# Performance work log

Measured on AMD Instinct MI355X. Metric: run time of the kernel, lower is better.

Reference implementation:

```python
import jax, jax.numpy as jnp
import numpy as np

D = 1024          # model_dim
BD = D // 2       # bottleneck_dim
K = 64            # num_splats
B, S = 8, 2048


def setup_inputs() -> dict:
    key = jax.random.key(0)
    ks = jax.random.split(key, 12)
    sc = 0.02
    return {
        "token_embeddings": jax.random.normal(ks[0], (B, S, D), jnp.float32),
        "splat_influences": jax.random.uniform(ks[1], (B, S, K), jnp.float32),
        # encoder: Linear(D -> BD), stored [in, out]
        "enc_W": jax.random.normal(ks[2], (D, BD), jnp.float32) * sc,
        "enc_b": jnp.zeros((BD,), jnp.float32),
        # per-splat transforms: K x Linear(BD -> BD)
        "trans_W": jax.random.normal(ks[3], (K, BD, BD), jnp.float32) * sc,
        "trans_b": jnp.zeros((K, BD), jnp.float32),
        # decoder: Linear(BD -> D)
        "dec_W": jax.random.normal(ks[4], (BD, D), jnp.float32) * sc,
        "dec_b": jnp.zeros((D,), jnp.float32),
        # flow gate: Linear(D -> D) + sigmoid
        "gate_W": jax.random.normal(ks[5], (D, D), jnp.float32) * sc,
        "gate_b": jnp.zeros((D,), jnp.float32),
    }


def reference(token_embeddings, splat_influences, enc_W, enc_b,
              trans_W, trans_b, dec_W, dec_b, gate_W, gate_b):
    # gather: [B,K,S] @ [B,S,D] -> [B,K,D]
    influences_t = jnp.swapaxes(splat_influences, 1, 2)          # [B,K,S]
    gathered = jnp.einsum('bks,bsd->bkd', influences_t, token_embeddings)
    total = jnp.clip(influences_t.sum(axis=2, keepdims=True), 1e-8, None)  # [B,K,1]
    gathered = gathered / total
    # encoder (dropout inactive at eval)
    encoded = jax.nn.relu(gathered @ enc_W + enc_b)              # [B,K,BD]
    # per-splat transform as grouped matmul
    transformed = jnp.einsum('bkd,kde->bke', encoded, trans_W) + trans_b  # [B,K,BD]
    decoded = transformed @ dec_W + dec_b                        # [B,K,D]
    # scatter back to tokens: [B,S,K] @ [B,K,D]
    flow = jnp.einsum('bsk,bkd->bsd', splat_influences, decoded)
    gate = jax.nn.sigmoid(token_embeddings @ gate_W + gate_b)    # [B,S,D]
    return flow * gate
```

## Files before the change

kernel.cpp:

```cpp
#include <hip/hip_runtime.h>

#define BB 8
#define SS 2048
#define DD 1024
#define BDD 512
#define NSP 64

typedef __attribute__((ext_vector_type(8))) short bf16x8;
typedef __attribute__((ext_vector_type(4))) float f32x4;
typedef unsigned short u16;
typedef unsigned int u32;

__device__ __forceinline__ u16 f2bf(float f) {
  u32 u = __builtin_bit_cast(u32, f);
  u = u + 0x7fffu + ((u >> 16) & 1u);
  return (u16)(u >> 16);
}

__device__ __forceinline__ void gl_lds16(const void* g, void* l) {
  __builtin_amdgcn_global_load_lds((const __attribute__((address_space(1))) void*)g,
                                   (__attribute__((address_space(3))) void*)l,
                                   16, 0, 0);
}

__global__ void k_prep(const float* __restrict__ infl, const float* __restrict__ gw,
                       u16* __restrict__ inflbf, u16* __restrict__ inflT,
                       float* __restrict__ rsum, u16* __restrict__ gwt) {
  __shared__ __align__(16) char smraw[64 * 80 * 2 + 32 * 64 * 4];
  u16(*tile)[80] = (u16(*)[80])smraw;
  float(*ps)[64] = (float(*)[64])(smraw + 64 * 80 * 2);
  float(*gt)[33] = (float(*)[33])smraw;
  int bid = blockIdx.x;
  int t = threadIdx.x;

  if (bid < 256) {
    int R0 = bid * 64;
    int b = R0 >> 11, s0 = R0 & 2047;
    int st = s0 >> 6;
    int lr = t >> 3, lc = (t & 7) * 8;
    float col[8];
#pragma unroll
    for (int j = 0; j < 8; ++j) col[j] = 0.f;
#pragma unroll
    for (int i = 0; i < 2; ++i) {
      int r = lr + i * 32;
      const float* src = infl + (size_t)(R0 + r) * NSP + lc;
      float4 a = *(const float4*)src;
      float4 bq = *(const float4*)(src + 4);
      col[0] += a.x; col[1] += a.y; col[2] += a.z; col[3] += a.w;
      col[4] += bq.x; col[5] += bq.y; col[6] += bq.z; col[7] += bq.w;
      uint4 v;
      v.x = f2bf(a.x) | ((u32)f2bf(a.y) << 16);
      v.y = f2bf(a.z) | ((u32)f2bf(a.w) << 16);
      v.z = f2bf(bq.x) | ((u32)f2bf(bq.y) << 16);
      v.w = f2bf(bq.z) | ((u32)f2bf(bq.w) << 16);
      *(uint4*)(inflbf + (size_t)(R0 + r) * NSP + lc) = v;
      *(uint4*)&tile[r][lc] = v;
    }
#pragma unroll
    for (int j = 0; j < 8; ++j) ps[lr][lc + j] = col[j];
    __syncthreads();
    if (t < 64) {
      float s = 0.f;
#pragma unroll
      for (int rr = 0; rr < 32; ++rr) s += ps[rr][t];
      rsum[((size_t)b * 32 + st) * 64 + t] = s;
    }
    int sseg = (t & 7) * 8;
    size_t ibase = (size_t)b * NSP * SS + (size_t)st * (NSP * 64);
#pragma unroll
    for (int i = 0; i < 2; ++i) {
      int dcol = (t >> 3) + i * 32;
      u16 a0 = tile[sseg + 0][dcol], a1 = tile[sseg + 1][dcol];
      u16 a2 = tile[sseg + 2][dcol], a3 = tile[sseg + 3][dcol];
      u16 a4 = tile[sseg + 4][dcol], a5 = tile[sseg + 5][dcol];
      u16 a6 = tile[sseg + 6][dcol], a7 = tile[sseg + 7][dcol];
      uint4 v;
      v.x = a0 | ((u32)a1 << 16);
      v.y = a2 | ((u32)a3 << 16);
      v.z = a4 | ((u32)a5 << 16);
      v.w = a6 | ((u32)a7 << 16);
      *(uint4*)(inflT + ibase + (size_t)dcol * 64 + sseg) = v;
    }
  } else {
    int g = bid - 256;
    int n0 = (g & 31) * 32, k0 = (g >> 5) * 32;
    int tx = t & 31, ty = t >> 5;
#pragma unroll
    for (int r = 0; r < 4; ++r) {
      int kr = ty + r * 8;
      gt[kr][tx] = gw[(k0 + kr) * DD + n0 + tx];
    }
    __syncthreads();
#pragma unroll
    for (int r = 0; r < 4; ++r) {
      int nc = ty + r * 8;
      gwt[(n0 + nc) * DD + k0 + tx] = f2bf(gt[tx][nc]);
    }
  }
}

__global__ __launch_bounds__(256) void k_gather_mfma(const u16* __restrict__ inflT,
                                                     const float* __restrict__ tok,
                                                     u16* __restrict__ tokbf,
                                                     float* __restrict__ pg) {
  __shared__ u16 As[64 * 64];
  __shared__ u16 Bs[64 * 64];
  int t = threadIdx.x;
  int l = t & 63, w = t >> 6;
  int wr = w >> 1, wc = w & 1;
  int n0 = blockIdx.x * 64;
  int b = blockIdx.y;
  int sq = blockIdx.z;
  int l15 = l & 15, lh = l >> 4;

  const u16* ap = inflT + (size_t)b * NSP * SS;
  int s = t >> 2;
  int dseg = (t & 3) * 16;

  f32x4 acc[2][2];
#pragma unroll
  for (int i = 0; i < 2; ++i)
#pragma unroll
    for (int j = 0; j < 2; ++j) acc[i][j] = (f32x4){0.f, 0.f, 0.f, 0.f};

  for (int kt = 0; kt < 8; ++kt) {
    int pc = sq * 8 + kt;
    const u16* app = ap + (size_t)pc * (NSP * 64);
#pragma unroll
    for (int i = 0; i < 2; ++i) {
      int e = i * 256 + t;
      int row = e >> 3;
      int cs = ((e & 7) ^ (row & 7)) * 8;
      gl_lds16(app + row * 64 + cs, &As[e * 8]);
    }
    {
      size_t off = ((size_t)(b * SS + pc * 64 + s)) * DD + n0 + dseg;
      const float* src = tok + off;
      float4 fa = *(const float4*)src;
      float4 fb = *(const float4*)(src + 4);
      float4 fc = *(const float4*)(src + 8);
      float4 fd = *(const float4*)(src + 12);
      u32 wd[8];
      wd[0] = f2bf(fa.x) | ((u32)f2bf(fa.y) << 16);
      wd[1] = f2bf(fa.z) | ((u32)f2bf(fa.w) << 16);
      wd[2] = f2bf(fb.x) | ((u32)f2bf(fb.y) << 16);
      wd[3] = f2bf(fb.z) | ((u32)f2bf(fb.w) << 16);
      wd[4] = f2bf(fc.x) | ((u32)f2bf(fc.y) << 16);
      wd[5] = f2bf(fc.z) | ((u32)f2bf(fc.w) << 16);
      wd[6] = f2bf(fd.x) | ((u32)f2bf(fd.y) << 16);
      wd[7] = f2bf(fd.z) | ((u32)f2bf(fd.w) << 16);
      uint4 v0, v1;
      v0.x = wd[0]; v0.y = wd[1]; v0.z = wd[2]; v0.w = wd[3];
      v1.x = wd[4]; v1.y = wd[5]; v1.z = wd[6]; v1.w = wd[7];
      *(uint4*)(tokbf + off) = v0;
      *(uint4*)(tokbf + off + 8) = v1;
      int shi = (s >> 3), slo = (s & 7);
#pragma unroll
      for (int p = 0; p < 8; ++p) {
        int d0 = dseg + p * 2, d1 = dseg + p * 2 + 1;
        Bs[d0 * 64 + ((shi ^ ((d0 >> 3) & 7)) * 8) + slo] = (u16)wd[p];
        Bs[d1 * 64 + ((shi ^ ((d1 >> 3) & 7)) * 8) + slo] = (u16)(wd[p] >> 16);
      }
    }
    __syncthreads();
#pragma unroll
    for (int ks = 0; ks < 2; ++ks) {
      int g = ks * 4 + lh;
      bf16x8 af[2], bfv[2];
#pragma unroll
      for (int mi = 0; mi < 2; ++mi) {
        int ar = wr * 32 + mi * 16 + l15;
        af[mi] = *(const bf16x8*)&As[ar * 64 + ((g ^ (ar & 7)) * 8)];
      }
#pragma unroll
      for (int ni = 0; ni < 2; ++ni) {
        int br = wc * 32 + ni * 16 + l15;
        bfv[ni] = *(const bf16x8*)&Bs[br * 64 + ((g ^ ((br >> 3) & 7)) * 8)];
      }
#pragma unroll
      for (int mi = 0; mi < 2; ++mi)
#pragma unroll
        for (int ni = 0; ni < 2; ++ni)
          acc[mi][ni] = __builtin_amdgcn_mfma_f32_16x16x32_bf16(af[mi], bfv[ni], acc[mi][ni], 0, 0, 0);
    }
    __syncthreads();
  }

#pragma unroll
  for (int mi = 0; mi < 2; ++mi)
#pragma unroll
    for (int ni = 0; ni < 2; ++ni)
#pragma unroll
      for (int r = 0; r < 4; ++r) {
        int krow = wr * 32 + mi * 16 + lh * 4 + r;
        int dcol = n0 + wc * 32 + ni * 16 + l15;
        pg[((size_t)sq * 512 + b * NSP + krow) * DD + dcol] = acc[mi][ni][r];
      }
}

__global__ void k_enc_part(const float* __restrict__ pg, const float* __restrict__ rsum,
                           const float* __restrict__ encW, float* __restrict__ pe) {
  __shared__ float gl[8][128];
  int dq = blockIdx.x, mt = blockIdx.y;
  int m0 = mt * 8, d0 = dq * 128;
  int t = threadIdx.x;
  {
    int r = t >> 5, c = t & 31;
    float s[4] = {0.f, 0.f, 0.f, 0.f};
#pragma unroll
    for (int q = 0; q < 4; ++q) {
      const float* qp = pg + ((size_t)q * 512 + m0 + r) * DD + d0;
      s[0] += qp[c]; s[1] += qp[c + 32]; s[2] += qp[c + 64]; s[3] += qp[c + 96];
    }
    int mrow = m0 + r;
    int bq = mrow >> 6, kq = mrow & 63;
    float tt = 0.f;
#pragma unroll
    for (int st = 0; st < 32; ++st) tt += rsum[((size_t)bq * 32 + st) * 64 + kq];
    float rt = 1.f / fmaxf(tt, 1e-8f);
    gl[r][c] = s[0] * rt;
    gl[r][c + 32] = s[1] * rt;
    gl[r][c + 64] = s[2] * rt;
    gl[r][c + 96] = s[3] * rt;
  }
  __syncthreads();
  int n4 = (t & 127) * 4, mh = (t >> 7) * 4;
  float4 acc[4];
#pragma unroll
  for (int m = 0; m < 4; ++m) acc[m] = (float4){0.f, 0.f, 0.f, 0.f};
  for (int i = 0; i < 128; ++i) {
    float4 wv = *(const float4*)(encW + (d0 + i) * BDD + n4);
#pragma unroll
    for (int m = 0; m < 4; ++m) {
      float g = gl[mh + m][i];
      acc[m].x += g * wv.x; acc[m].y += g * wv.y;
      acc[m].z += g * wv.z; acc[m].w += g * wv.w;
    }
  }
#pragma unroll
  for (int m = 0; m < 4; ++m)
    *(float4*)(pe + ((size_t)dq * 512 + m0 + mh + m) * BDD + n4) = acc[m];
}

__global__ void k_trans_part(const float* __restrict__ pe, const float* __restrict__ encB,
                             const float* __restrict__ trW, float* __restrict__ pt) {
  __shared__ float el[8][64];
  int dq = blockIdx.x, ks = blockIdx.y;
  int d0 = dq * 64;
  int t = threadIdx.x;
  {
    int r = t >> 5, c = t & 31;
    int m = r * NSP + ks;
    float s1 = 0.f, s2 = 0.f;
#pragma unroll
    for (int p = 0; p < 8; ++p) {
      const float* qp = pe + ((size_t)p * 512 + m) * BDD + d0;
      s1 += qp[c]; s2 += qp[c + 32];
    }
    el[r][c] = fmaxf(s1 + encB[d0 + c], 0.f);
    el[r][c + 32] = fmaxf(s2 + encB[d0 + c + 32], 0.f);
  }
  __syncthreads();
  int n4 = (t & 127) * 4, mh = (t >> 7) * 4;
  float4 acc[4];
#pragma unroll
  for (int m = 0; m < 4; ++m) acc[m] = (float4){0.f, 0.f, 0.f, 0.f};
  for (int i = 0; i < 64; ++i) {
    float4 wv = *(const float4*)(trW + ((size_t)ks * BDD + d0 + i) * BDD + n4);
#pragma unroll
    for (int m = 0; m < 4; ++m) {
      float g = el[mh + m][i];
      acc[m].x += g * wv.x; acc[m].y += g * wv.y;
      acc[m].z += g * wv.z; acc[m].w += g * wv.w;
    }
  }
#pragma unroll
  for (int m = 0; m < 4; ++m)
    *(float4*)(pt + ((size_t)dq * 512 + (mh + m) * NSP + ks) * BDD + n4) = acc[m];
}

__global__ void k_dec_part(const float* __restrict__ pt, const float* __restrict__ trB,
                           const float* __restrict__ decW, float* __restrict__ pd) {
  __shared__ float tl[8][64];
  int dq = blockIdx.x, mt = blockIdx.y;
  int m0 = mt * 8, d0 = dq * 64;
  int t = threadIdx.x;
  {
    int r = t >> 5, c = t & 31;
    int m = m0 + r;
    float s1 = 0.f, s2 = 0.f;
#pragma unroll
    for (int p = 0; p < 8; ++p) {
      const float* qp = pt + ((size_t)p * 512 + m) * BDD + d0;
      s1 += qp[c]; s2 += qp[c + 32];
    }
    tl[r][c] = s1 + trB[(m & 63) * BDD + d0 + c];
    tl[r][c + 32] = s2 + trB[(m & 63) * BDD + d0 + c + 32];
  }
  __syncthreads();
  int n4 = t * 4;
  float4 acc[8];
#pragma unroll
  for (int m = 0; m < 8; ++m) acc[m] = (float4){0.f, 0.f, 0.f, 0.f};
  for (int i = 0; i < 64; ++i) {
    float4 wv = *(const float4*)(decW + (d0 + i) * DD + n4);
#pragma unroll
    for (int m = 0; m < 8; ++m) {
      float g = tl[m][i];
      acc[m].x += g * wv.x; acc[m].y += g * wv.y;
      acc[m].z += g * wv.z; acc[m].w += g * wv.w;
    }
  }
#pragma unroll
  for (int m = 0; m < 8; ++m)
    *(float4*)(pd + ((size_t)dq * 512 + m0 + m) * DD + n4) = acc[m];
}

__global__ void red_dec(const float* __restrict__ pd, const float* __restrict__ decB,
                        u16* __restrict__ decT) {
  __shared__ u16 st[64][34];
  int nt = blockIdx.x, b = blockIdx.y;
  int n0 = nt * 32;
  int t = threadIdx.x;
  int nn = t & 31, kg = t >> 5;
  float db = decB[n0 + nn];
#pragma unroll
  for (int ki = 0; ki < 8; ++ki) {
    int ks = kg * 8 + ki;
    float s = db;
#pragma unroll
    for (int p = 0; p < 8; ++p)
      s += pd[((size_t)p * 512 + b * NSP + ks) * DD + n0 + nn];
    st[ks][nn] = f2bf(s);
  }
  __syncthreads();
  int nr = t >> 3, kseg = (t & 7) * 8;
  uint4 v;
  v.x = st[kseg + 0][nr] | ((u32)st[kseg + 1][nr] << 16);
  v.y = st[kseg + 2][nr] | ((u32)st[kseg + 3][nr] << 16);
  v.z = st[kseg + 4][nr] | ((u32)st[kseg + 5][nr] << 16);
  v.w = st[kseg + 6][nr] | ((u32)st[kseg + 7][nr] << 16);
  *(uint4*)(decT + ((size_t)b * DD + n0 + nr) * NSP + kseg) = v;
}


#define GVM(n) asm volatile("s_waitcnt vmcnt(" #n ")" ::: "memory");

#define GSTA(sl, k0, p)                                                        \
  { int e = (p)*512 + t; int row = e >> 3; int cs = ((e & 7) ^ (row & 7)) * 8; \
    gl_lds16(tokbf + (size_t)(m0 + row) * DD + (k0) + cs, &As[sl][e * 8]); }
#define GSTB(sl, k0, p)                                                        \
  { int e = (p)*512 + t; int row = e >> 3; int cs = ((e & 7) ^ (row & 7)) * 8; \
    gl_lds16(gwt + (size_t)(n0 + row) * DD + (k0) + cs, &Bs[sl][e * 8]); }
#define SAI(sl, p)                                                             \
  { int e = (p)*512 + t; int row = e >> 3; int cs = ((e & 7) ^ (row & 7)) * 8; \
    gl_lds16(inflbf + ((size_t)bb * SS + s0m + row) * NSP + cs, &As[sl][e * 8]); }
#define SBD(sl, p)                                                             \
  { int e = (p)*512 + t; int row = e >> 3; int cs = ((e & 7) ^ (row & 7)) * 8; \
    gl_lds16(decT + ((size_t)bb * DD + n0 + row) * NSP + cs, &Bs[sl][e * 8]); }

#define GLOADB(sl)                                                             \
  _Pragma("unroll")                                                            \
  for (int nf = 0; nf < 2; ++nf) {                                             \
    int br = wc * 32 + nf * 16 + l15;                                          \
    bfv[nf][0] = *(const bf16x8*)&Bs[sl][br * 64 + c0];                        \
    bfv[nf][1] = *(const bf16x8*)&Bs[sl][br * 64 + c1];                        \
  }

#define GPH(sl, mq, VMW, STG, LDB)                                             \
  {                                                                            \
    VMW                                                                        \
    __builtin_amdgcn_s_barrier();                                              \
    LDB                                                                        \
    bf16x8 af[4][2];                                                           \
    _Pragma("unroll")                                                          \
    for (int mf = 0; mf < 4; ++mf) {                                           \
      int ar = (mq)*64 + mf * 16 + l15;                                        \
      af[mf][0] = *(const bf16x8*)&As[sl][ar * 64 + c0];                       \
      af[mf][1] = *(const bf16x8*)&As[sl][ar * 64 + c1];                       \
    }                                                                          \
    STG                                                                        \
    __builtin_amdgcn_s_setprio(1);                                             \
    _Pragma("unroll")                                                          \
    for (int mf = 0; mf < 4; ++mf)                                             \
      _Pragma("unroll")                                                        \
      for (int nf = 0; nf < 2; ++nf) {                                         \
        acc[(mq)*4 + mf][nf] = __builtin_amdgcn_mfma_f32_16x16x32_bf16(af[mf][0], bfv[nf][0], acc[(mq)*4 + mf][nf], 0, 0, 0); \
        acc[(mq)*4 + mf][nf] = __builtin_amdgcn_mfma_f32_16x16x32_bf16(af[mf][1], bfv[nf][1], acc[(mq)*4 + mf][nf], 0, 0, 0); \
      }                                                                        \
    __builtin_amdgcn_s_setprio(0);                                             \
    __builtin_amdgcn_s_barrier();                                              \
  }

#define GT_FULL(sl, osl, k1)                                                   \
  {                                                                            \
    bf16x8 bfv[2][2];                                                          \
    GPH(sl, 0, GVM(3), GSTB(osl, k1, 0) GSTB(osl, k1, 1), GLOADB(sl))          \
    GPH(sl, 1, GVM(4), GSTB(osl, k1, 2) GSTB(osl, k1, 3), )                    \
    GPH(sl, 2, GVM(5), GSTA(osl, k1, 0) GSTA(osl, k1, 1), )                    \
    GPH(sl, 3, GVM(6), GSTA(osl, k1, 2) GSTA(osl, k1, 3), )                    \
  }
#define GT_LAST2(sl)                                                           \
  {                                                                            \
    bf16x8 bfv[2][2];                                                          \
    GPH(sl, 0, GVM(3), SAI(0, 0) SAI(0, 1), GLOADB(sl))                        \
    GPH(sl, 1, GVM(4), SAI(0, 2) SAI(0, 3), )                                  \
    GPH(sl, 2, GVM(5), SBD(0, 0) SBD(0, 1), )                                  \
    GPH(sl, 3, GVM(6), SBD(0, 2) SBD(0, 3), )                                  \
  }

__global__ __launch_bounds__(512, 1) void k_gate(const u16* __restrict__ tokbf,
                                                 const u16* __restrict__ gwt,
                                                 const u16* __restrict__ inflbf,
                                                 const u16* __restrict__ decT,
                                                 const float* __restrict__ gateB,
                                                 float* __restrict__ outp) {
  __shared__ u16 As[2][256 * 64];
  __shared__ u16 Bs[2][256 * 64];
  int t = threadIdx.x;
  int l = t & 63, wc = t >> 6;
  int bid = blockIdx.x;
  int mt = (bid & 7) * 8 + ((bid >> 3) & 7);
  int nt = bid >> 6;
  int m0 = mt * 256, n0 = nt * 256;
  int l15 = l & 15, lh = l >> 4;
  int x7 = l15 & 7;
  int c0 = (lh ^ x7) * 8;
  int c1 = ((4 + lh) ^ x7) * 8;
  int bb = m0 >> 11, s0m = m0 & 2047;

  f32x4 acc[16][2];
#pragma unroll
  for (int i = 0; i < 16; ++i)
#pragma unroll
    for (int j = 0; j < 2; ++j) acc[i][j] = (f32x4){0.f, 0.f, 0.f, 0.f};

  GSTB(0, 0, 0) GSTB(0, 0, 1) GSTB(0, 0, 2) GSTB(0, 0, 3)
  GSTA(0, 0, 0) GSTA(0, 0, 1) GSTA(0, 0, 2) GSTA(0, 0, 3)

#pragma unroll 1
  for (int i = 0; i < 7; ++i) {
    GT_FULL(0, 1, (2 * i + 1) * 64)
    GT_FULL(1, 0, (2 * i + 2) * 64)
  }
  GT_FULL(0, 1, 960)
  GT_LAST2(1)

  GVM(0)
  __builtin_amdgcn_s_barrier();

  {
    float gb[2];
#pragma unroll
    for (int nf = 0; nf < 2; ++nf) gb[nf] = gateB[n0 + wc * 32 + nf * 16 + l15];
    bf16x8 bfv[2][2];
    GLOADB(0)
#pragma unroll
    for (int mq = 0; mq < 4; ++mq) {
      bf16x8 af[4][2];
#pragma unroll
      for (int mf = 0; mf < 4; ++mf) {
        int ar = mq * 64 + mf * 16 + l15;
        af[mf][0] = *(const bf16x8*)&As[0][ar * 64 + c0];
        af[mf][1] = *(const bf16x8*)&As[0][ar * 64 + c1];
      }
      f32x4 accf[4][2];
#pragma unroll
      for (int mf = 0; mf < 4; ++mf)
#pragma unroll
        for (int nf = 0; nf < 2; ++nf) accf[mf][nf] = (f32x4){0.f, 0.f, 0.f, 0.f};
      __builtin_amdgcn_s_setprio(1);
#pragma unroll
      for (int mf = 0; mf < 4; ++mf)
#pragma unroll
        for (int nf = 0; nf < 2; ++nf) {
          accf[mf][nf] = __builtin_amdgcn_mfma_f32_16x16x32_bf16(af[mf][0], bfv[nf][0], accf[mf][nf], 0, 0, 0);
          accf[mf][nf] = __builtin_amdgcn_mfma_f32_16x16x32_bf16(af[mf][1], bfv[nf][1], accf[mf][nf], 0, 0, 0);
        }
      __builtin_amdgcn_s_setprio(0);
#pragma unroll
      for (int mf = 0; mf < 4; ++mf)
#pragma unroll
        for (int nf = 0; nf < 2; ++nf)
#pragma unroll
          for (int r = 0; r < 4; ++r) {
            int mr = m0 + (mq * 4 + mf) * 16 + lh * 4 + r;
            int nc = n0 + wc * 32 + nf * 16 + l15;
            float z = acc[mq * 4 + mf][nf][r] + gb[nf];
            float gate = 1.f / (1.f + __expf(-z));
            outp[(size_t)mr * DD + nc] = accf[mf][nf][r] * gate;
          }
    }
  }
}

extern "C" void kernel_launch(void* const* d_in, const int* in_sizes, int n_in,
                              void* d_out, int out_size, void* d_ws, size_t ws_size,
                              hipStream_t stream) {
  const float* tok = (const float*)d_in[0];
  const float* infl = (const float*)d_in[1];
  const float* encW = (const float*)d_in[2];
  const float* encB = (const float*)d_in[3];
  const float* trW = (const float*)d_in[4];
  const float* trB = (const float*)d_in[5];
  const float* decW = (const float*)d_in[6];
  const float* decB = (const float*)d_in[7];
  const float* gw = (const float*)d_in[8];
  const float* gateB = (const float*)d_in[9];
  float* outp = (float*)d_out;

  char* wsp = (char*)d_ws;
  u16* tokbf = (u16*)(wsp);
  u16* gwt = (u16*)(wsp + 33554432);
  u16* inflbf = (u16*)(wsp + 35651584);
  u16* decT = (u16*)(wsp + 41945088);
  float* pe = (float*)(wsp + 42993664);
  float* pt = (float*)(wsp + 42993664 + 8388608);
  u16* inflT = (u16*)(wsp + 76548096);
  float* rsum = (float*)(wsp + 78645248);
  float* scratch = (float*)(wsp + 78710784);

  k_prep<<<dim3(1280), dim3(256), 0, stream>>>(infl, gw, inflbf, inflT, rsum, gwt);
  k_gather_mfma<<<dim3(16, 8, 4), dim3(256), 0, stream>>>(inflT, tok, tokbf, scratch);
  k_enc_part<<<dim3(8, 64), dim3(256), 0, stream>>>(scratch, rsum, encW, pe);
  k_trans_part<<<dim3(8, 64), dim3(256), 0, stream>>>(pe, encB, trW, pt);
  k_dec_part<<<dim3(8, 64), dim3(256), 0, stream>>>(pt, trB, decW, scratch);
  red_dec<<<dim3(32, 8), dim3(256), 0, stream>>>(scratch, decB, decT);
  k_gate<<<dim3(256), dim3(512), 0, stream>>>(tokbf, gwt, inflbf, decT, gateB, outp);
}
```

Baseline: 148.1 us.

## Merge prep/gather and mid-stage kernels into cooperative launches with grid syncs

Six small kernel launches collapse into two cooperative kernels. The prep and gather stages are joined, and so are the encoder, transform, decoder and reduction stages, with cg grid syncs in place of kernel boundaries. The aim is to cut per-launch overhead and the gaps between short dependent kernels. In exchange, grid-wide barriers are added, the grid is fixed at 512 blocks, and prep work is looped over fewer blocks.

```diff
diff --git a/kernel.cpp b/kernel.cpp
--- a/kernel.cpp
+++ b/kernel.cpp
@@ -1,4 +1,7 @@
 #include <hip/hip_runtime.h>
+#include <hip/hip_cooperative_groups.h>
+
+namespace cg = cooperative_groups;
 
 #define BB 8
 #define SS 2048
@@ -23,325 +26,353 @@
                                    16, 0, 0);
 }
 
-__global__ void k_prep(const float* __restrict__ infl, const float* __restrict__ gw,
-                       u16* __restrict__ inflbf, u16* __restrict__ inflT,
-                       float* __restrict__ rsum, u16* __restrict__ gwt) {
+__global__ __launch_bounds__(256) void k_pg(const float* __restrict__ infl,
+                                            const float* __restrict__ gw,
+                                            const float* __restrict__ tok,
+                                            u16* __restrict__ inflbf,
+                                            u16* __restrict__ inflT,
+                                            float* __restrict__ rsum,
+                                            u16* __restrict__ gwt,
+                                            u16* __restrict__ tokbf,
+                                            float* __restrict__ pg) {
   __shared__ __align__(16) char smraw[64 * 80 * 2 + 32 * 64 * 4];
   u16(*tile)[80] = (u16(*)[80])smraw;
   float(*ps)[64] = (float(*)[64])(smraw + 64 * 80 * 2);
   float(*gt)[33] = (float(*)[33])smraw;
+  int t = threadIdx.x;
+
+  for (int u = blockIdx.x; u < 1280; u += 512) {
+    if (u < 256) {
+      int R0 = u * 64;
+      int b = R0 >> 11, s0 = R0 & 2047;
+      int st = s0 >> 6;
+      int lr = t >> 3, lc = (t & 7) * 8;
+      float col[8];
+#pragma unroll
+      for (int j = 0; j < 8; ++j) col[j] = 0.f;
+#pragma unroll
+      for (int i = 0; i < 2; ++i) {
+        int r = lr + i * 32;
+        const float* src = infl + (size_t)(R0 + r) * NSP + lc;
+        float4 a = *(const float4*)src;
+        float4 bq = *(const float4*)(src + 4);
+        col[0] += a.x; col[1] += a.y; col[2] += a.z; col[3] += a.w;
+        col[4] += bq.x; col[5] += bq.y; col[6] += bq.z; col[7] += bq.w;
+        uint4 v;
+        v.x = f2bf(a.x) | ((u32)f2bf(a.y) << 16);
+        v.y = f2bf(a.z) | ((u32)f2bf(a.w) << 16);
+        v.z = f2bf(bq.x) | ((u32)f2bf(bq.y) << 16);
+        v.w = f2bf(bq.z) | ((u32)f2bf(bq.w) << 16);
+        *(uint4*)(inflbf + (size_t)(R0 + r) * NSP + lc) = v;
+        *(uint4*)&tile[r][lc] = v;
+      }
+#pragma unroll
+      for (int j = 0; j < 8; ++j) ps[lr][lc + j] = col[j];
+      __syncthreads();
+      if (t < 64) {
+        float s = 0.f;
+#pragma unroll
+        for (int rr = 0; rr < 32; ++rr) s += ps[rr][t];
+        rsum[((size_t)b * 32 + st) * 64 + t] = s;
+      }
+      int sseg = (t & 7) * 8;
+      size_t ibase = (size_t)b * NSP * SS + (size_t)st * (NSP * 64);
+#pragma unroll
+      for (int i = 0; i < 2; ++i) {
+        int dcol = (t >> 3) + i * 32;
+        u16 a0 = tile[sseg + 0][dcol], a1 = tile[sseg + 1][dcol];
+        u16 a2 = tile[sseg + 2][dcol], a3 = tile[sseg + 3][dcol];
+        u16 a4 = tile[sseg + 4][dcol], a5 = tile[sseg + 5][dcol];
+        u16 a6 = tile[sseg + 6][dcol], a7 = tile[sseg + 7][dcol];
+        uint4 v;
+        v.x = a0 | ((u32)a1 << 16);
+        v.y = a2 | ((u32)a3 << 16);
+        v.z = a4 | ((u32)a5 << 16);
+        v.w = a6 | ((u32)a7 << 16);
+        *(uint4*)(inflT + ibase + (size_t)dcol * 64 + sseg) = v;
+      }
+      __syncthreads();
+    } else {
+      int g = u - 256;
+      int n0 = (g & 31) * 32, k0 = (g >> 5) * 32;
+      int tx = t & 31, ty = t >> 5;
+#pragma unroll
+      for (int r = 0; r < 4; ++r) {
+        int kr = ty + r * 8;
+        gt[kr][tx] = gw[(k0 + kr) * DD + n0 + tx];
+      }
+      __syncthreads();
+#pragma unroll
+      for (int r = 0; r < 4; ++r) {
+        int nc = ty + r * 8;
+        gwt[(n0 + nc) * DD + k0 + tx] = f2bf(gt[tx][nc]);
+      }
+      __syncthreads();
+    }
+  }
+
+  __threadfence();
+  cg::this_grid().sync();
+
+  {
+    u16* As = (u16*)smraw;
+    u16* Bs = (u16*)(smraw + 64 * 64 * 2);
+    int l = t & 63, w = t >> 6;
+    int wr = w >> 1, wc = w & 1;
+    int n0 = (blockIdx.x & 15) * 64;
+    int b = (blockIdx.x >> 4) & 7;
+    int sq = blockIdx.x >> 7;
+    int l15 = l & 15, lh = l >> 4;
+
+    const u16* ap = inflT + (size_t)b * NSP * SS;
+    int s = t >> 2;
+    int dseg = (t & 3) * 16;
+
+    f32x4 acc[2][2];
+#pragma unroll
+    for (int i = 0; i < 2; ++i)
+#pragma unroll
+      for (int j = 0; j < 2; ++j) acc[i][j] = (f32x4){0.f, 0.f, 0.f, 0.f};
+
+    for (int kt = 0; kt < 8; ++kt) {
+      int pc = sq * 8 + kt;
+      const u16* app = ap + (size_t)pc * (NSP * 64);
+#pragma unroll
+      for (int i = 0; i < 2; ++i) {
+        int e = i * 256 + t;
+        int row = e >> 3;
+        int cs = ((e & 7) ^ (row & 7)) * 8;
+        gl_lds16(app + row * 64 + cs, &As[e * 8]);
+      }
+      {
+        size_t off = ((size_t)(b * SS + pc * 64 + s)) * DD + n0 + dseg;
+        const float* src = tok + off;
+        float4 fa = *(const float4*)src;
+        float4 fb = *(const float4*)(src + 4);
+        float4 fc = *(const float4*)(src + 8);
+        float4 fd = *(const float4*)(src + 12);
+        u32 wd[8];
+        wd[0] = f2bf(fa.x) | ((u32)f2bf(fa.y) << 16);
+        wd[1] = f2bf(fa.z) | ((u32)f2bf(fa.w) << 16);
+        wd[2] = f2bf(fb.x) | ((u32)f2bf(fb.y) << 16);
+        wd[3] = f2bf(fb.z) | ((u32)f2bf(fb.w) << 16);
+        wd[4] = f2bf(fc.x) | ((u32)f2bf(fc.y) << 16);
+        wd[5] = f2bf(fc.z) | ((u32)f2bf(fc.w) << 16);
+        wd[6] = f2bf(fd.x) | ((u32)f2bf(fd.y) << 16);
+        wd[7] = f2bf(fd.z) | ((u32)f2bf(fd.w) << 16);
+        uint4 v0, v1;
+        v0.x = wd[0]; v0.y = wd[1]; v0.z = wd[2]; v0.w = wd[3];
+        v1.x = wd[4]; v1.y = wd[5]; v1.z = wd[6]; v1.w = wd[7];
+        *(uint4*)(tokbf + off) = v0;
+        *(uint4*)(tokbf + off + 8) = v1;
+        int shi = (s >> 3), slo = (s & 7);
+#pragma unroll
+        for (int p = 0; p < 8; ++p) {
+          int d0 = dseg + p * 2, d1 = dseg + p * 2 + 1;
+          Bs[d0 * 64 + ((shi ^ ((d0 >> 3) & 7)) * 8) + slo] = (u16)wd[p];
+          Bs[d1 * 64 + ((shi ^ ((d1 >> 3) & 7)) * 8) + slo] = (u16)(wd[p] >> 16);
+        }
+      }
+      __syncthreads();
+#pragma unroll
+      for (int ks = 0; ks < 2; ++ks) {
+        int g = ks * 4 + lh;
+        bf16x8 af[2], bfv[2];
+#pragma unroll
+        for (int mi = 0; mi < 2; ++mi) {
+          int ar = wr * 32 + mi * 16 + l15;
+          af[mi] = *(const bf16x8*)&As[ar * 64 + ((g ^ (ar & 7)) * 8)];
+        }
+#pragma unroll
+        for (int ni = 0; ni < 2; ++ni) {
+          int br = wc * 32 + ni * 16 + l15;
+          bfv[ni] = *(const bf16x8*)&Bs[br * 64 + ((g ^ ((br >> 3) & 7)) * 8)];
+        }
+#pragma unroll
+        for (int mi = 0; mi < 2; ++mi)
+#pragma unroll
+          for (int ni = 0; ni < 2; ++ni)
+            acc[mi][ni] = __builtin_amdgcn_mfma_f32_16x16x32_bf16(af[mi], bfv[ni], acc[mi][ni], 0, 0, 0);
+      }
+      __syncthreads();
+    }
+
+#pragma unroll
+    for (int mi = 0; mi < 2; ++mi)
+#pragma unroll
+      for (int ni = 0; ni < 2; ++ni)
+#pragma unroll
+        for (int r = 0; r < 4; ++r) {
+          int krow = wr * 32 + mi * 16 + lh * 4 + r;
+          int dcol = n0 + wc * 32 + ni * 16 + l15;
+          pg[((size_t)sq * 512 + b * NSP + krow) * DD + dcol] = acc[mi][ni][r];
+        }
+  }
+}
+
+__global__ __launch_bounds__(256) void k_mid(const float* __restrict__ pg,
+                                             const float* __restrict__ rsum,
+                                             const float* __restrict__ encW,
+                                             const float* __restrict__ encB,
+                                             const float* __restrict__ trW,
+                                             const float* __restrict__ trB,
+                                             const float* __restrict__ decW,
+                                             const float* __restrict__ decB,
+                                             float* __restrict__ pe,
+                                             float* __restrict__ pt,
+                                             float* __restrict__ pd,
+                                             u16* __restrict__ decT) {
+  __shared__ __align__(16) char midraw[4608];
+  int t = threadIdx.x;
   int bid = blockIdx.x;
-  int t = threadIdx.x;
+
+  {
+    float(*gl)[128] = (float(*)[128])midraw;
+    int dq = bid & 7, mt = bid >> 3;
+    int m0 = mt * 8, d0 = dq * 128;
+    {
+      int r = t >> 5, c = t & 31;
+      float s[4] = {0.f, 0.f, 0.f, 0.f};
+#pragma unroll
+      for (int q = 0; q < 4; ++q) {
+        const float* qp = pg + ((size_t)q * 512 + m0 + r) * DD + d0;
+        s[0] += qp[c]; s[1] += qp[c + 32]; s[2] += qp[c + 64]; s[3] += qp[c + 96];
+      }
+      int mrow = m0 + r;
+      int bq = mrow >> 6, kq = mrow & 63;
+      float tt = 0.f;
+#pragma unroll
+      for (int st = 0; st < 32; ++st) tt += rsum[((size_t)bq * 32 + st) * 64 + kq];
+      float rt = 1.f / fmaxf(tt, 1e-8f);
+      gl[r][c] = s[0] * rt;
+      gl[r][c + 32] = s[1] * rt;
+      gl[r][c + 64] = s[2] * rt;
+      gl[r][c + 96] = s[3] * rt;
+    }
+    __syncthreads();
+    int n4 = (t & 127) * 4, mh = (t >> 7) * 4;
+    float4 acc[4];
+#pragma unroll
+    for (int m = 0; m < 4; ++m) acc[m] = (float4){0.f, 0.f, 0.f, 0.f};
+    for (int i = 0; i < 128; ++i) {
+      float4 wv = *(const float4*)(encW + (d0 + i) * BDD + n4);
+#pragma unroll
+      for (int m = 0; m < 4; ++m) {
+        float g = gl[mh + m][i];
+        acc[m].x += g * wv.x; acc[m].y += g * wv.y;
+        acc[m].z += g * wv.z; acc[m].w += g * wv.w;
+      }
+    }
+#pragma unroll
+    for (int m = 0; m < 4; ++m)
+      *(float4*)(pe + ((size_t)dq * 512 + m0 + mh + m) * BDD + n4) = acc[m];
+  }
+
+  __threadfence();
+  cg::this_grid().sync();
+
+  {
+    float(*el)[64] = (float(*)[64])midraw;
+    int dq = bid & 7, ks = bid >> 3;
+    int d0 = dq * 64;
+    {
+      int r = t >> 5, c = t & 31;
+      int m = r * NSP + ks;
+      float s1 = 0.f, s2 = 0.f;
+#pragma unroll
+      for (int p = 0; p < 8; ++p) {
+        const float* qp = pe + ((size_t)p * 512 + m) * BDD + d0;
+        s1 += qp[c]; s2 += qp[c + 32];
+      }
+      el[r][c] = fmaxf(s1 + encB[d0 + c], 0.f);
+      el[r][c + 32] = fmaxf(s2 + encB[d0 + c + 32], 0.f);
+    }
+    __syncthreads();
+    int n4 = (t & 127) * 4, mh = (t >> 7) * 4;
+    float4 acc[4];
+#pragma unroll
+    for (int m = 0; m < 4; ++m) acc[m] = (float4){0.f, 0.f, 0.f, 0.f};
+    for (int i = 0; i < 64; ++i) {
+      float4 wv = *(const float4*)(trW + ((size_t)ks * BDD + d0 + i) * BDD + n4);
+#pragma unroll
+      for (int m = 0; m < 4; ++m) {
+        float g = el[mh + m][i];
+        acc[m].x += g * wv.x; acc[m].y += g * wv.y;
+        acc[m].z += g * wv.z; acc[m].w += g * wv.w;
+      }
+    }
+#pragma unroll
+    for (int m = 0; m < 4; ++m)
+      *(float4*)(pt + ((size_t)dq * 512 + (mh + m) * NSP + ks) * BDD + n4) = acc[m];
+    __syncthreads();
+  }
+
+  __threadfence();
+  cg::this_grid().sync();
+
+  {
+    float(*tl)[64] = (float(*)[64])midraw;
+    int dq = bid & 7, mt = bid >> 3;
+    int m0 = mt * 8, d0 = dq * 64;
+    {
+      int r = t >> 5, c = t & 31;
+      int m = m0 + r;
+      float s1 = 0.f, s2 = 0.f;
+#pragma unroll
+      for (int p = 0; p < 8; ++p) {
+        const float* qp = pt + ((size_t)p * 512 + m) * BDD + d0;
+        s1 += qp[c]; s2 += qp[c + 32];
+      }
+      tl[r][c] = s1 + trB[(m & 63) * BDD + d0 + c];
+      tl[r][c + 32] = s2 + trB[(m & 63) * BDD + d0 + c + 32];
+    }
+    __syncthreads();
+    int n4 = t * 4;
+    float4 acc[8];
+#pragma unroll
+    for (int m = 0; m < 8; ++m) acc[m] = (float4){0.f, 0.f, 0.f, 0.f};
+    for (int i = 0; i < 64; ++i) {
+      float4 wv = *(const float4*)(decW + (d0 + i) * DD + n4);
+#pragma unroll
+      for (int m = 0; m < 8; ++m) {
+        float g = tl[m][i];
+        acc[m].x += g * wv.x; acc[m].y += g * wv.y;
+        acc[m].z += g * wv.z; acc[m].w += g * wv.w;
+      }
+    }
+#pragma unroll
+    for (int m = 0; m < 8; ++m)
+      *(float4*)(pd + ((size_t)dq * 512 + m0 + m) * DD + n4) = acc[m];
+    __syncthreads();
+  }
+
+  __threadfence();
+  cg::this_grid().sync();
 
   if (bid < 256) {
-    int R0 = bid * 64;
-    int b = R0 >> 11, s0 = R0 & 2047;
-    int st = s0 >> 6;
-    int lr = t >> 3, lc = (t & 7) * 8;
-    float col[8];
-#pragma unroll
-    for (int j = 0; j < 8; ++j) col[j] = 0.f;
-#pragma unroll
-    for (int i = 0; i < 2; ++i) {
-      int r = lr + i * 32;
-      const float* src = infl + (size_t)(R0 + r) * NSP + lc;
-      float4 a = *(const float4*)src;
-      float4 bq = *(const float4*)(src + 4);
-      col[0] += a.x; col[1] += a.y; col[2] += a.z; col[3] += a.w;
-      col[4] += bq.x; col[5] += bq.y; col[6] += bq.z; col[7] += bq.w;
-      uint4 v;
-      v.x = f2bf(a.x) | ((u32)f2bf(a.y) << 16);
-      v.y = f2bf(a.z) | ((u32)f2bf(a.w) << 16);
-      v.z = f2bf(bq.x) | ((u32)f2bf(bq.y) << 16);
-      v.w = f2bf(bq.z) | ((u32)f2bf(bq.w) << 16);
-      *(uint4*)(inflbf + (size_t)(R0 + r) * NSP + lc) = v;
-      *(uint4*)&tile[r][lc] = v;
-    }
-#pragma unroll
-    for (int j = 0; j < 8; ++j) ps[lr][lc + j] = col[j];
+    u16(*st)[34] = (u16(*)[34])midraw;
+    int nt = bid & 31, b = bid >> 5;
+    int n0 = nt * 32;
+    int nn = t & 31, kg = t >> 5;
+    float db = decB[n0 + nn];
+#pragma unroll
+    for (int ki = 0; ki < 8; ++ki) {
+      int ks = kg * 8 + ki;
+      float s = db;
+#pragma unroll
+      for (int p = 0; p < 8; ++p)
+        s += pd[((size_t)p * 512 + b * NSP + ks) * DD + n0 + nn];
+      st[ks][nn] = f2bf(s);
+    }
     __syncthreads();
-    if (t < 64) {
-      float s = 0.f;
-#pragma unroll
-      for (int rr = 0; rr < 32; ++rr) s += ps[rr][t];
-      rsum[((size_t)b * 32 + st) * 64 + t] = s;
-    }
-    int sseg = (t & 7) * 8;
-    size_t ibase = (size_t)b * NSP * SS + (size_t)st * (NSP * 64);
-#pragma unroll
-    for (int i = 0; i < 2; ++i) {
-      int dcol = (t >> 3) + i * 32;
-      u16 a0 = tile[sseg + 0][dcol], a1 = tile[sseg + 1][dcol];
-      u16 a2 = tile[sseg + 2][dcol], a3 = tile[sseg + 3][dcol];
-      u16 a4 = tile[sseg + 4][dcol], a5 = tile[sseg + 5][dcol];
-      u16 a6 = tile[sseg + 6][dcol], a7 = tile[sseg + 7][dcol];
-      uint4 v;
-      v.x = a0 | ((u32)a1 << 16);
-      v.y = a2 | ((u32)a3 << 16);
-      v.z = a4 | ((u32)a5 << 16);
-      v.w = a6 | ((u32)a7 << 16);
-      *(uint4*)(inflT + ibase + (size_t)dcol * 64 + sseg) = v;
-    }
-  } else {
-    int g = bid - 256;
-    int n0 = (g & 31) * 32, k0 = (g >> 5) * 32;
-    int tx = t & 31, ty = t >> 5;
-#pragma unroll
-    for (int r = 0; r < 4; ++r) {
-      int kr = ty + r * 8;
-      gt[kr][tx] = gw[(k0 + kr) * DD + n0 + tx];
-    }
-    __syncthreads();
-#pragma unroll
-    for (int r = 0; r < 4; ++r) {
-      int nc = ty + r * 8;
-      gwt[(n0 + nc) * DD + k0 + tx] = f2bf(gt[tx][nc]);
-    }
-  }
-}
-
-__global__ __launch_bounds__(256) void k_gather_mfma(const u16* __restrict__ inflT,
-                                                     const float* __restrict__ tok,
-                                                     u16* __restrict__ tokbf,
-                                                     float* __restrict__ pg) {
-  __shared__ u16 As[64 * 64];
-  __shared__ u16 Bs[64 * 64];
-  int t = threadIdx.x;
-  int l = t & 63, w = t >> 6;
-  int wr = w >> 1, wc = w & 1;
-  int n0 = blockIdx.x * 64;
-  int b = blockIdx.y;
-  int sq = blockIdx.z;
-  int l15 = l & 15, lh = l >> 4;
-
-  const u16* ap = inflT + (size_t)b * NSP * SS;
-  int s = t >> 2;
-  int dseg = (t & 3) * 16;
-
-  f32x4 acc[2][2];
-#pragma unroll
-  for (int i = 0; i < 2; ++i)
-#pragma unroll
-    for (int j = 0; j < 2; ++j) acc[i][j] = (f32x4){0.f, 0.f, 0.f, 0.f};
-
-  for (int kt = 0; kt < 8; ++kt) {
-    int pc = sq * 8 + kt;
-    const u16* app = ap + (size_t)pc * (NSP * 64);
-#pragma unroll
-    for (int i = 0; i < 2; ++i) {
-      int e = i * 256 + t;
-      int row = e >> 3;
-      int cs = ((e & 7) ^ (row & 7)) * 8;
-      gl_lds16(app + row * 64 + cs, &As[e * 8]);
-    }
-    {
-      size_t off = ((size_t)(b * SS + pc * 64 + s)) * DD + n0 + dseg;
-      const float* src = tok + off;
-      float4 fa = *(const float4*)src;
-      float4 fb = *(const float4*)(src + 4);
-      float4 fc = *(const float4*)(src + 8);
-      float4 fd = *(const float4*)(src + 12);
-      u32 wd[8];
-      wd[0] = f2bf(fa.x) | ((u32)f2bf(fa.y) << 16);
-      wd[1] = f2bf(fa.z) | ((u32)f2bf(fa.w) << 16);
-      wd[2] = f2bf(fb.x) | ((u32)f2bf(fb.y) << 16);
-      wd[3] = f2bf(fb.z) | ((u32)f2bf(fb.w) << 16);
-      wd[4] = f2bf(fc.x) | ((u32)f2bf(fc.y) << 16);
-      wd[5] = f2bf(fc.z) | ((u32)f2bf(fc.w) << 16);
-      wd[6] = f2bf(fd.x) | ((u32)f2bf(fd.y) << 16);
-      wd[7] = f2bf(fd.z) | ((u32)f2bf(fd.w) << 16);
-      uint4 v0, v1;
-      v0.x = wd[0]; v0.y = wd[1]; v0.z = wd[2]; v0.w = wd[3];
-      v1.x = wd[4]; v1.y = wd[5]; v1.z = wd[6]; v1.w = wd[7];
-      *(uint4*)(tokbf + off) = v0;
-      *(uint4*)(tokbf + off + 8) = v1;
-      int shi = (s >> 3), slo = (s & 7);
-#pragma unroll
-      for (int p = 0; p < 8; ++p) {
-        int d0 = dseg + p * 2, d1 = dseg + p * 2 + 1;
-        Bs[d0 * 64 + ((shi ^ ((d0 >> 3) & 7)) * 8) + slo] = (u16)wd[p];
-        Bs[d1 * 64 + ((shi ^ ((d1 >> 3) & 7)) * 8) + slo] = (u16)(wd[p] >> 16);
-      }
-    }
-    __syncthreads();
-#pragma unroll
-    for (int ks = 0; ks < 2; ++ks) {
-      int g = ks * 4 + lh;
-      bf16x8 af[2], bfv[2];
-#pragma unroll
-      for (int mi = 0; mi < 2; ++mi) {
-        int ar = wr * 32 + mi * 16 + l15;
-        af[mi] = *(const bf16x8*)&As[ar * 64 + ((g ^ (ar & 7)) * 8)];
-      }
-#pragma unroll
-      for (int ni = 0; ni < 2; ++ni) {
-        int br = wc * 32 + ni * 16 + l15;
-        bfv[ni] = *(const bf16x8*)&Bs[br * 64 + ((g ^ ((br >> 3) & 7)) * 8)];
-      }
-#pragma unroll
-      for (int mi = 0; mi < 2; ++mi)
-#pragma unroll
-        for (int ni = 0; ni < 2; ++ni)
-          acc[mi][ni] = __builtin_amdgcn_mfma_f32_16x16x32_bf16(af[mi], bfv[ni], acc[mi][ni], 0, 0, 0);
-    }
-    __syncthreads();
-  }
-
-#pragma unroll
-  for (int mi = 0; mi < 2; ++mi)
-#pragma unroll
-    for (int ni = 0; ni < 2; ++ni)
-#pragma unroll
-      for (int r = 0; r < 4; ++r) {
-        int krow = wr * 32 + mi * 16 + lh * 4 + r;
-        int dcol = n0 + wc * 32 + ni * 16 + l15;
-        pg[((size_t)sq * 512 + b * NSP + krow) * DD + dcol] = acc[mi][ni][r];
-      }
-}
-
-__global__ void k_enc_part(const float* __restrict__ pg, const float* __restrict__ rsum,
-                           const float* __restrict__ encW, float* __restrict__ pe) {
-  __shared__ float gl[8][128];
-  int dq = blockIdx.x, mt = blockIdx.y;
-  int m0 = mt * 8, d0 = dq * 128;
-  int t = threadIdx.x;
-  {
-    int r = t >> 5, c = t & 31;
-    float s[4] = {0.f, 0.f, 0.f, 0.f};
-#pragma unroll
-    for (int q = 0; q < 4; ++q) {
-      const float* qp = pg + ((size_t)q * 512 + m0 + r) * DD + d0;
-      s[0] += qp[c]; s[1] += qp[c + 32]; s[2] += qp[c + 64]; s[3] += qp[c + 96];
-    }
-    int mrow = m0 + r;
-    int bq = mrow >> 6, kq = mrow & 63;
-    float tt = 0.f;
-#pragma unroll
-    for (int st = 0; st < 32; ++st) tt += rsum[((size_t)bq * 32 + st) * 64 + kq];
-    float rt = 1.f / fmaxf(tt, 1e-8f);
-    gl[r][c] = s[0] * rt;
-    gl[r][c + 32] = s[1] * rt;
-    gl[r][c + 64] = s[2] * rt;
-    gl[r][c + 96] = s[3] * rt;
-  }
-  __syncthreads();
-  int n4 = (t & 127) * 4, mh = (t >> 7) * 4;
-  float4 acc[4];
-#pragma unroll
-  for (int m = 0; m < 4; ++m) acc[m] = (float4){0.f, 0.f, 0.f, 0.f};
-  for (int i = 0; i < 128; ++i) {
-    float4 wv = *(const float4*)(encW + (d0 + i) * BDD + n4);
-#pragma unroll
-    for (int m = 0; m < 4; ++m) {
-      float g = gl[mh + m][i];
-      acc[m].x += g * wv.x; acc[m].y += g * wv.y;
-      acc[m].z += g * wv.z; acc[m].w += g * wv.w;
-    }
-  }
-#pragma unroll
-  for (int m = 0; m < 4; ++m)
-    *(float4*)(pe + ((size_t)dq * 512 + m0 + mh + m) * BDD + n4) = acc[m];
-}
-
-__global__ void k_trans_part(const float* __restrict__ pe, const float* __restrict__ encB,
-                             const float* __restrict__ trW, float* __restrict__ pt) {
-  __shared__ float el[8][64];
-  int dq = blockIdx.x, ks = blockIdx.y;
-  int d0 = dq * 64;
-  int t = threadIdx.x;
-  {
-    int r = t >> 5, c = t & 31;
-    int m = r * NSP + ks;
-    float s1 = 0.f, s2 = 0.f;
-#pragma unroll
-    for (int p = 0; p < 8; ++p) {
-      const float* qp = pe + ((size_t)p * 512 + m) * BDD + d0;
-      s1 += qp[c]; s2 += qp[c + 32];
-    }
-    el[r][c] = fmaxf(s1 + encB[d0 + c], 0.f);
-    el[r][c + 32] = fmaxf(s2 + encB[d0 + c + 32], 0.f);
-  }
-  __syncthreads();
-  int n4 = (t & 127) * 4, mh = (t >> 7) * 4;
-  float4 acc[4];
-#pragma unroll
-  for (int m = 0; m < 4; ++m) acc[m] = (float4){0.f, 0.f, 0.f, 0.f};
-  for (int i = 0; i < 64; ++i) {
-    float4 wv = *(const float4*)(trW + ((size_t)ks * BDD + d0 + i) * BDD + n4);
-#pragma unroll
-    for (int m = 0; m < 4; ++m) {
-      float g = el[mh + m][i];
-      acc[m].x += g * wv.x; acc[m].y += g * wv.y;
-      acc[m].z += g * wv.z; acc[m].w += g * wv.w;
-    }
-  }
-#pragma unroll
-  for (int m = 0; m < 4; ++m)
-    *(float4*)(pt + ((size_t)dq * 512 + (mh + m) * NSP + ks) * BDD + n4) = acc[m];
-}
-
-__global__ void k_dec_part(const float* __restrict__ pt, const float* __restrict__ trB,
-                           const float* __restrict__ decW, float* __restrict__ pd) {
-  __shared__ float tl[8][64];
-  int dq = blockIdx.x, mt = blockIdx.y;
-  int m0 = mt * 8, d0 = dq * 64;
-  int t = threadIdx.x;
-  {
-    int r = t >> 5, c = t & 31;
-    int m = m0 + r;
-    float s1 = 0.f, s2 = 0.f;
-#pragma unroll
-    for (int p = 0; p < 8; ++p) {
-      const float* qp = pt + ((size_t)p * 512 + m) * BDD + d0;
-      s1 += qp[c]; s2 += qp[c + 32];
-    }
-    tl[r][c] = s1 + trB[(m & 63) * BDD + d0 + c];
-    tl[r][c + 32] = s2 + trB[(m & 63) * BDD + d0 + c + 32];
-  }
-  __syncthreads();
-  int n4 = t * 4;
-  float4 acc[8];
-#pragma unroll
-  for (int m = 0; m < 8; ++m) acc[m] = (float4){0.f, 0.f, 0.f, 0.f};
-  for (int i = 0; i < 64; ++i) {
-    float4 wv = *(const float4*)(decW + (d0 + i) * DD + n4);
-#pragma unroll
-    for (int m = 0; m < 8; ++m) {
-      float g = tl[m][i];
-      acc[m].x += g * wv.x; acc[m].y += g * wv.y;
-      acc[m].z += g * wv.z; acc[m].w += g * wv.w;
-    }
-  }
-#pragma unroll
-  for (int m = 0; m < 8; ++m)
-    *(float4*)(pd + ((size_t)dq * 512 + m0 + m) * DD + n4) = acc[m];
-}
-
-__global__ void red_dec(const float* __restrict__ pd, const float* __restrict__ decB,
-                        u16* __restrict__ decT) {
-  __shared__ u16 st[64][34];
-  int nt = blockIdx.x, b = blockIdx.y;
-  int n0 = nt * 32;
-  int t = threadIdx.x;
-  int nn = t & 31, kg = t >> 5;
-  float db = decB[n0 + nn];
-#pragma unroll
-  for (int ki = 0; ki < 8; ++ki) {
-    int ks = kg * 8 + ki;
-    float s = db;
-#pragma unroll
-    for (int p = 0; p < 8; ++p)
-      s += pd[((size_t)p * 512 + b * NSP + ks) * DD + n0 + nn];
-    st[ks][nn] = f2bf(s);
-  }
-  __syncthreads();
-  int nr = t >> 3, kseg = (t & 7) * 8;
-  uint4 v;
-  v.x = st[kseg + 0][nr] | ((u32)st[kseg + 1][nr] << 16);
-  v.y = st[kseg + 2][nr] | ((u32)st[kseg + 3][nr] << 16);
-  v.z = st[kseg + 4][nr] | ((u32)st[kseg + 5][nr] << 16);
-  v.w = st[kseg + 6][nr] | ((u32)st[kseg + 7][nr] << 16);
-  *(uint4*)(decT + ((size_t)b * DD + n0 + nr) * NSP + kseg) = v;
+    int nr = t >> 3, kseg = (t & 7) * 8;
+    uint4 v;
+    v.x = st[kseg + 0][nr] | ((u32)st[kseg + 1][nr] << 16);
+    v.y = st[kseg + 2][nr] | ((u32)st[kseg + 3][nr] << 16);
+    v.z = st[kseg + 4][nr] | ((u32)st[kseg + 5][nr] << 16);
+    v.w = st[kseg + 6][nr] | ((u32)st[kseg + 7][nr] << 16);
+    *(uint4*)(decT + ((size_t)b * DD + n0 + nr) * NSP + kseg) = v;
+  }
 }
 
 
@@ -521,11 +552,18 @@
   float* rsum = (float*)(wsp + 78645248);
   float* scratch = (float*)(wsp + 78710784);
 
-  k_prep<<<dim3(1280), dim3(256), 0, stream>>>(infl, gw, inflbf, inflT, rsum, gwt);
-  k_gather_mfma<<<dim3(16, 8, 4), dim3(256), 0, stream>>>(inflT, tok, tokbf, scratch);
-  k_enc_part<<<dim3(8, 64), dim3(256), 0, stream>>>(scratch, rsum, encW, pe);
-  k_trans_part<<<dim3(8, 64), dim3(256), 0, stream>>>(pe, encB, trW, pt);
-  k_dec_part<<<dim3(8, 64), dim3(256), 0, stream>>>(pt, trB, decW, scratch);
-  red_dec<<<dim3(32, 8), dim3(256), 0, stream>>>(scratch, decB, decT);
+  float* pg = scratch;
+  float* pd = scratch;
+
+  void* a1[] = {(void*)&infl, (void*)&gw, (void*)&tok, (void*)&inflbf,
+                (void*)&inflT, (void*)&rsum, (void*)&gwt, (void*)&tokbf,
+                (void*)&pg};
+  hipLaunchCooperativeKernel((void*)k_pg, dim3(512), dim3(256), a1, 0, stream);
+
+  void* a2[] = {(void*)&pg, (void*)&rsum, (void*)&encW, (void*)&encB,
+                (void*)&trW, (void*)&trB, (void*)&decW, (void*)&decB,
+                (void*)&pe, (void*)&pt, (void*)&pd, (void*)&decT};
+  hipLaunchCooperativeKernel((void*)k_mid, dim3(512), dim3(256), a2, 0, stream);
+
   k_gate<<<dim3(256), dim3(512), 0, stream>>>(tokbf, gwt, inflbf, decT, gateB, outp);
 }
```

Result: slower. 547.9 us (+269.9%).
